# Performance work log

Hardware: AMD Instinct MI355X
Metric: run time of the kernel (lower is better)

## Reference

```python
import jax, jax.numpy as jnp
import numpy as np

N_NODES = 50000
N_EDGES = 800000
D_IN = 128
D_HID = 128
N_CLASSES = 10
N_GRAPHS = 64


def setup_inputs() -> dict:
    key = jax.random.key(0)
    ks = jax.random.split(key, 12)
    x = jax.random.normal(ks[0], (N_NODES, D_IN), dtype=jnp.float32)
    edge_index = jax.random.randint(ks[1], (2, N_EDGES), 0, N_NODES, dtype=jnp.int32)
    batch = jnp.sort(jax.random.randint(ks[2], (N_NODES,), 0, N_GRAPHS, dtype=jnp.int32))
    s = 0.05
    conv0_w = jax.random.normal(ks[3], (D_IN, D_HID), dtype=jnp.float32) * s
    conv0_b = jax.random.normal(ks[4], (D_HID,), dtype=jnp.float32) * s
    conv1_w = jax.random.normal(ks[5], (D_HID, D_HID), dtype=jnp.float32) * s
    conv1_b = jax.random.normal(ks[6], (D_HID,), dtype=jnp.float32) * s
    lin0_w = jax.random.normal(ks[7], (D_HID, D_HID), dtype=jnp.float32) * s
    lin0_b = jax.random.normal(ks[8], (D_HID,), dtype=jnp.float32) * s
    lin1_w = jax.random.normal(ks[9], (D_HID, N_CLASSES), dtype=jnp.float32) * s
    lin1_b = jax.random.normal(ks[10], (N_CLASSES,), dtype=jnp.float32) * s
    return dict(x=x, edge_index=edge_index, batch=batch,
                conv0_w=conv0_w, conv0_b=conv0_b,
                conv1_w=conv1_w, conv1_b=conv1_b,
                lin0_w=lin0_w, lin0_b=lin0_b,
                lin1_w=lin1_w, lin1_b=lin1_b)


def gcn_conv(x, edge_index, w, b):
    # PyG GCNConv: linear transform, add self-loops, D^-1/2 (A+I) D^-1/2 aggregation, + bias
    n = x.shape[0]
    h = x @ w  # [N, out]
    loop = jnp.arange(n, dtype=edge_index.dtype)
    row = jnp.concatenate([edge_index[0], loop])  # source nodes
    col = jnp.concatenate([edge_index[1], loop])  # destination nodes
    deg = jax.ops.segment_sum(jnp.ones_like(col, dtype=h.dtype), col, num_segments=n)
    dinv = jnp.where(deg > 0, jax.lax.rsqrt(deg), 0.0)
    norm = dinv[row] * dinv[col]  # [E+N]
    msg = h[row] * norm[:, None]  # gather + scale
    out = jax.ops.segment_sum(msg, col, num_segments=n)  # scatter-add
    return out + b


def reference(x, edge_index, batch, conv0_w, conv0_b, conv1_w, conv1_b,
              lin0_w, lin0_b, lin1_w, lin1_b):
    h = jax.nn.relu(gcn_conv(x, edge_index, conv0_w, conv0_b))
    h = jax.nn.relu(gcn_conv(h, edge_index, conv1_w, conv1_b))
    # global max pooling over nodes of each graph
    h = jax.ops.segment_max(h, batch, num_segments=N_GRAPHS)  # [G, D_HID]
    # NOTE: original applies relu after EVERY linear, including the output layer
    h = jax.nn.relu(h @ lin0_w + lin0_b)
    h = jax.nn.relu(h @ lin1_w + lin1_b)
    return jax.nn.log_softmax(h, axis=-1)
```

## Files before the change

### kernel.cpp

```cpp
#include <hip/hip_runtime.h>

#define D 128
#define BINCAP 6144
#define P2CAP 6144

typedef __attribute__((ext_vector_type(8))) short short8;
typedef __attribute__((ext_vector_type(4))) float f32x4;
typedef __attribute__((ext_vector_type(2))) float f32x2;

__device__ inline unsigned short f2bf(float f) {
    unsigned u = __float_as_uint(f);
    return (unsigned short)((u + 0x7FFFu + ((u >> 16) & 1u)) >> 16);
}
__device__ inline float bflo(unsigned u) { return __uint_as_float(u << 16); }
__device__ inline float bfhi(unsigned u) { return __uint_as_float(u & 0xFFFF0000u); }

__global__ __launch_bounds__(256) void k_initW(const float* __restrict__ w0, const float* __restrict__ w1,
                                               const float* __restrict__ b0, const float* __restrict__ b1,
                                               uint4* __restrict__ Wp0, uint4* __restrict__ Wp1,
                                               float* __restrict__ b0p, float* __restrict__ b1p,
                                               int* __restrict__ binCur, int* __restrict__ pool,
                                               unsigned* __restrict__ h0b, unsigned* __restrict__ h1b,
                                               int nbins, int n) {
    int t = threadIdx.x, b = blockIdx.x;
    int e = b * 256 + t;
    {
        int l = e & 63, U = (e >> 6) & 7, T = e >> 9;
        int nn = U * 16 + (l & 15);
        int kq = T * 32 + ((l >> 4) << 3);
        unsigned r[4], s[4];
#pragma unroll
        for (int jj = 0; jj < 4; ++jj) {
            int k0 = kq + 2 * jj, k1 = k0 + 1;
            unsigned a0 = f2bf(w0[k0 * 128 + nn]), a1 = f2bf(w0[k1 * 128 + nn]);
            r[jj] = a0 | (a1 << 16);
            int c0 = ((k0 & 7) << 4) | (k0 >> 3), c1 = ((k1 & 7) << 4) | (k1 >> 3);
            unsigned q0 = f2bf(w1[c0 * 128 + nn]), q1 = f2bf(w1[c1 * 128 + nn]);
            s[jj] = q0 | (q1 << 16);
        }
        Wp0[e] = make_uint4(r[0], r[1], r[2], r[3]);
        Wp1[e] = make_uint4(s[0], s[1], s[2], s[3]);
    }
    if (b == 0) {
        if (t < nbins) binCur[t] = t * BINCAP;
        for (int i = t; i < 64 * 128; i += 256) pool[i] = 0;
    }
    if (b == 1 && t < 128) {
        int c = ((t & 7) << 4) | (t >> 3);
        b0p[t] = b0[c];
        b1p[t] = b1[c];
    }
    if (b == 2 && t < 64) {
        h0b[(size_t)n * 64 + t] = 0u;
        h1b[(size_t)n * 64 + t] = 0u;
    }
}

__global__ __launch_bounds__(256) void k_p1scatter(const int* __restrict__ row, const int* __restrict__ col,
                                                   int* __restrict__ binCur, unsigned* __restrict__ ebuf, int E) {
    __shared__ int h[256], delta[256], lcur[256], wt[4];
    __shared__ unsigned stage[4096];
    int t = threadIdx.x;
    int wv = t >> 6, l = t & 63;
    h[t] = 0;
    __syncthreads();
    int base = blockIdx.x * 4096;
    int cnt = min(4096, E - base);
    if (cnt == 4096) {
        int myc[16], myr[16];
        const int4* c4 = (const int4*)(col + base);
        const int4* r4 = (const int4*)(row + base);
#pragma unroll
        for (int k = 0; k < 4; ++k) {
            int4 cv = c4[t * 4 + k];
            int4 rv = r4[t * 4 + k];
            myc[k * 4 + 0] = cv.x; myc[k * 4 + 1] = cv.y; myc[k * 4 + 2] = cv.z; myc[k * 4 + 3] = cv.w;
            myr[k * 4 + 0] = rv.x; myr[k * 4 + 1] = rv.y; myr[k * 4 + 2] = rv.z; myr[k * 4 + 3] = rv.w;
        }
#pragma unroll
        for (int k = 0; k < 16; ++k) atomicAdd(&h[myc[k] >> 8], 1);
        __syncthreads();
        int v = h[t];
        int inc = v;
#pragma unroll
        for (int o = 1; o < 64; o <<= 1) {
            int x = __shfl_up(inc, o, 64);
            if (l >= o) inc += x;
        }
        if (l == 63) wt[wv] = inc;
        __syncthreads();
        int wbase = 0;
#pragma unroll
        for (int j = 0; j < 4; ++j) if (j < wv) wbase += wt[j];
        int excl = wbase + inc - v;
        lcur[t] = excl;
        delta[t] = (v > 0) ? (atomicAdd(&binCur[t], v) - excl) : 0;
        __syncthreads();
#pragma unroll
        for (int k = 0; k < 16; ++k) {
            int d = myc[k];
            int slot = atomicAdd(&lcur[d >> 8], 1);
            stage[slot] = ((unsigned)d << 16) | (unsigned)myr[k];
        }
        __syncthreads();
#pragma unroll
        for (int k = 0; k < 16; ++k) {
            int slot = k * 256 + t;
            unsigned vv = stage[slot];
            int b = vv >> 24;
            ebuf[delta[b] + slot] = vv;
        }
    } else {
        for (int k = 0; k < 16; ++k) {
            int e = base + k * 256 + t;
            if (e < E) atomicAdd(&h[col[e] >> 8], 1);
        }
        __syncthreads();
        int v = h[t];
        int inc = v;
#pragma unroll
        for (int o = 1; o < 64; o <<= 1) {
            int x = __shfl_up(inc, o, 64);
            if (l >= o) inc += x;
        }
        if (l == 63) wt[wv] = inc;
        __syncthreads();
        int wbase = 0;
#pragma unroll
        for (int j = 0; j < 4; ++j) if (j < wv) wbase += wt[j];
        int excl = wbase + inc - v;
        lcur[t] = excl;
        delta[t] = (v > 0) ? (atomicAdd(&binCur[t], v) - excl) : 0;
        __syncthreads();
        for (int k = 0; k < 16; ++k) {
            int e = base + k * 256 + t;
            if (e < E) {
                int d = col[e];
                int slot = atomicAdd(&lcur[d >> 8], 1);
                stage[slot] = ((unsigned)d << 16) | (unsigned)row[e];
            }
        }
        __syncthreads();
        for (int k = 0; k < 16; ++k) {
            int slot = k * 256 + t;
            if (slot < cnt) {
                unsigned vv = stage[slot];
                int b = vv >> 24;
                ebuf[delta[b] + slot] = vv;
            }
        }
    }
}

__global__ __launch_bounds__(256) void k_p2sort(const unsigned* __restrict__ ebuf, const int* __restrict__ binCur,
                                                int* __restrict__ csr, int* __restrict__ off_, int* __restrict__ end_,
                                                float* __restrict__ dinv, int n) {
    __shared__ unsigned stage[P2CAP];
    __shared__ unsigned stage2[P2CAP];
    __shared__ int h[256], cur[256], wt[4];
    int b = blockIdx.x, t = threadIdx.x;
    int wv = t >> 6, l = t & 63;
    int beg = b * BINCAP;
    int cnt = binCur[b] - beg;
    h[t] = 0;
    __syncthreads();
    int nfull = cnt >> 2;
    const uint4* e4 = (const uint4*)(ebuf + beg);
    uint4* st4 = (uint4*)stage;
    for (int i = t; i < nfull; i += 256) {
        uint4 v = e4[i];
        st4[i] = v;
        atomicAdd(&h[(v.x >> 16) & 0xFF], 1);
        atomicAdd(&h[(v.y >> 16) & 0xFF], 1);
        atomicAdd(&h[(v.z >> 16) & 0xFF], 1);
        atomicAdd(&h[(v.w >> 16) & 0xFF], 1);
    }
    for (int i = (nfull << 2) + t; i < cnt; i += 256) {
        unsigned v = ebuf[beg + i];
        stage[i] = v;
        atomicAdd(&h[(v >> 16) & 0xFF], 1);
    }
    __syncthreads();
    int v = h[t];
    int inc = v;
#pragma unroll
    for (int o = 1; o < 64; o <<= 1) {
        int x = __shfl_up(inc, o, 64);
        if (l >= o) inc += x;
    }
    if (l == 63) wt[wv] = inc;
    __syncthreads();
    int wbase = 0;
#pragma unroll
    for (int j = 0; j < 4; ++j) if (j < wv) wbase += wt[j];
    int excl = wbase + inc - v;
    cur[t] = excl;
    int d = b * 256 + t;
    if (d < n) {
        off_[d] = beg + excl;
        end_[d] = beg + excl + v;
        dinv[d] = rsqrtf((float)(v + 1));
    }
    __syncthreads();
    for (int i = t; i < cnt; i += 256) {
        unsigned vv = stage[i];
        int slot = atomicAdd(&cur[(vv >> 16) & 0xFF], 1);
        stage2[slot] = vv & 0xFFFFu;
    }
    __syncthreads();
    uint4* c4o = (uint4*)(csr + beg);
    uint4* st24 = (uint4*)stage2;
    for (int i = t; i < nfull; i += 256) c4o[i] = st24[i];
    for (int i = (nfull << 2) + t; i < cnt; i += 256) csr[beg + i] = (int)stage2[i];
}

__global__ __launch_bounds__(256) void k_gemm0(const float* __restrict__ x, const uint4* __restrict__ Wp,
                                               const float* __restrict__ dinv, unsigned* __restrict__ outb, int n) {
    int wave = threadIdx.x >> 6, l = threadIdx.x & 63;
    int mt = blockIdx.x * 4 + wave;
    int r0 = mt * 16;
    if (r0 >= n) return;
    int rowA = r0 + (l & 15);
    int kq = (l >> 4) * 8;
    f32x4 acc[8];
#pragma unroll
    for (int U = 0; U < 8; ++U) acc[U] = (f32x4){0.f, 0.f, 0.f, 0.f};
    const float* xr = x + (size_t)rowA * 128 + kq;
#pragma unroll
    for (int T = 0; T < 4; ++T) {
        float4 a0 = *(const float4*)(xr + T * 32);
        float4 a1 = *(const float4*)(xr + T * 32 + 4);
        short8 af;
        af[0] = (short)f2bf(a0.x); af[1] = (short)f2bf(a0.y);
        af[2] = (short)f2bf(a0.z); af[3] = (short)f2bf(a0.w);
        af[4] = (short)f2bf(a1.x); af[5] = (short)f2bf(a1.y);
        af[6] = (short)f2bf(a1.z); af[7] = (short)f2bf(a1.w);
#pragma unroll
        for (int U = 0; U < 8; ++U) {
            short8 bf = *(const short8*)&Wp[(T * 8 + U) * 64 + l];
            acc[U] = __builtin_amdgcn_mfma_f32_16x16x32_bf16(af, bf, acc[U], 0, 0, 0);
        }
    }
    int rq = l >> 4, cl = l & 15;
#pragma unroll
    for (int q = 0; q < 4; ++q) {
        int rr = r0 + rq * 4 + q;
        float d = dinv[rr];
        uint4 w;
        w.x = (unsigned)f2bf(acc[0][q] * d) | ((unsigned)f2bf(acc[1][q] * d) << 16);
        w.y = (unsigned)f2bf(acc[2][q] * d) | ((unsigned)f2bf(acc[3][q] * d) << 16);
        w.z = (unsigned)f2bf(acc[4][q] * d) | ((unsigned)f2bf(acc[5][q] * d) << 16);
        w.w = (unsigned)f2bf(acc[6][q] * d) | ((unsigned)f2bf(acc[7][q] * d) << 16);
        *(uint4*)(outb + (size_t)rr * 64 + cl * 4) = w;
    }
}

__device__ inline void gather8(const uint4* __restrict__ hp4, const int* __restrict__ csr,
                               int q, int beg, int len, int ZR, f32x2 acc[4]) {
    int maxlen = len;
    maxlen = max(maxlen, __shfl_xor(maxlen, 16, 64));
    maxlen = max(maxlen, __shfl_xor(maxlen, 32, 64));
    if (maxlen <= 0) return;
    int lm1 = len - 1;
    int s[8];
#pragma unroll
    for (int k = 0; k < 8; ++k) {
        int cv = csr[beg + min(k, lm1)];
        s[k] = (k < len) ? cv : ZR;
    }
    for (int j = 0; j < maxlen; j += 8) {
        uint4 u0 = hp4[(size_t)s[0] * 16 + q];
        uint4 u1 = hp4[(size_t)s[1] * 16 + q];
        uint4 u2 = hp4[(size_t)s[2] * 16 + q];
        uint4 u3 = hp4[(size_t)s[3] * 16 + q];
        uint4 u4 = hp4[(size_t)s[4] * 16 + q];
        uint4 u5 = hp4[(size_t)s[5] * 16 + q];
        uint4 u6 = hp4[(size_t)s[6] * 16 + q];
        uint4 u7 = hp4[(size_t)s[7] * 16 + q];
        int jn = j + 8;
        if (jn < maxlen) {
#pragma unroll
            for (int k = 0; k < 8; ++k) {
                int cv = csr[beg + min(jn + k, lm1)];
                s[k] = (jn + k < len) ? cv : ZR;
            }
        }
#define ACC8(U)                                                     \
        { f32x2 t0, t1, t2, t3;                                     \
          t0[0] = bflo(U.x); t0[1] = bfhi(U.x);                     \
          t1[0] = bflo(U.y); t1[1] = bfhi(U.y);                     \
          t2[0] = bflo(U.z); t2[1] = bfhi(U.z);                     \
          t3[0] = bflo(U.w); t3[1] = bfhi(U.w);                     \
          acc[0] += t0; acc[1] += t1; acc[2] += t2; acc[3] += t3; }
        ACC8(u0) ACC8(u1) ACC8(u2) ACC8(u3)
        ACC8(u4) ACC8(u5) ACC8(u6) ACC8(u7)
#undef ACC8
    }
}

__global__ __launch_bounds__(256) void k_aggemm(const unsigned* __restrict__ hp, const int* __restrict__ off_,
                                                const int* __restrict__ end_, const int* __restrict__ csr,
                                                const float* __restrict__ dinv, const float* __restrict__ bp,
                                                const uint4* __restrict__ Wp, unsigned* __restrict__ outb, int n) {
    __shared__ uint4 sA[16 * 17];
    int w = threadIdx.x >> 6, l = threadIdx.x & 63;
    int g = l >> 4, q = l & 15;
    int r0 = blockIdx.x * 16;
    int node = r0 + w * 4 + g;
    const uint4* hp4 = (const uint4*)hp;
    f32x2 acc[4];
    uint4 us = hp4[(size_t)node * 16 + q];
    acc[0][0] = bflo(us.x); acc[0][1] = bfhi(us.x);
    acc[1][0] = bflo(us.y); acc[1][1] = bfhi(us.y);
    acc[2][0] = bflo(us.z); acc[2][1] = bfhi(us.z);
    acc[3][0] = bflo(us.w); acc[3][1] = bfhi(us.w);
    int beg = off_[node];
    int len = end_[node] - beg;
    gather8(hp4, csr, q, beg, len, n, acc);
    float d0 = dinv[node];
    const float4* bp4 = (const float4*)bp;
    float4 ba = bp4[q * 2], bb = bp4[q * 2 + 1];
    uint4 pk;
    pk.x = (unsigned)f2bf(fmaxf(fmaf(d0, acc[0][0], ba.x), 0.f)) | ((unsigned)f2bf(fmaxf(fmaf(d0, acc[0][1], ba.y), 0.f)) << 16);
    pk.y = (unsigned)f2bf(fmaxf(fmaf(d0, acc[1][0], ba.z), 0.f)) | ((unsigned)f2bf(fmaxf(fmaf(d0, acc[1][1], ba.w), 0.f)) << 16);
    pk.z = (unsigned)f2bf(fmaxf(fmaf(d0, acc[2][0], bb.x), 0.f)) | ((unsigned)f2bf(fmaxf(fmaf(d0, acc[2][1], bb.y), 0.f)) << 16);
    pk.w = (unsigned)f2bf(fmaxf(fmaf(d0, acc[3][0], bb.z), 0.f)) | ((unsigned)f2bf(fmaxf(fmaf(d0, acc[3][1], bb.w), 0.f)) << 16);
    sA[(w * 4 + g) * 17 + q] = pk;
    __syncthreads();
    int rq = l >> 4, cl = l & 15;
    f32x4 c0v = (f32x4){0.f, 0.f, 0.f, 0.f}, c1v = (f32x4){0.f, 0.f, 0.f, 0.f};
#pragma unroll
    for (int T = 0; T < 4; ++T) {
        short8 af = *(const short8*)&sA[(l & 15) * 17 + T * 4 + rq];
        short8 bf0 = *(const short8*)&Wp[(T * 8 + 2 * w) * 64 + l];
        short8 bf1 = *(const short8*)&Wp[(T * 8 + 2 * w + 1) * 64 + l];
        c0v = __builtin_amdgcn_mfma_f32_16x16x32_bf16(af, bf0, c0v, 0, 0, 0);
        c1v = __builtin_amdgcn_mfma_f32_16x16x32_bf16(af, bf1, c1v, 0, 0, 0);
    }
#pragma unroll
    for (int qq = 0; qq < 4; ++qq) {
        int rr = r0 + rq * 4 + qq;
        float d2 = dinv[rr];
        unsigned pkk = (unsigned)f2bf(c0v[qq] * d2) | ((unsigned)f2bf(c1v[qq] * d2) << 16);
        outb[(size_t)rr * 64 + cl * 4 + w] = pkk;
    }
}

__global__ __launch_bounds__(256) void k_agg1(const unsigned* __restrict__ hp, const int* __restrict__ off_,
                                              const int* __restrict__ end_, const int* __restrict__ csr,
                                              const float* __restrict__ dinv, const float* __restrict__ bp,
                                              const int* __restrict__ batch, int* __restrict__ pool, int n) {
    __shared__ float2 sv[16][64];
    __shared__ int sg[16];
    int w = threadIdx.x >> 6, l = threadIdx.x & 63;
    int g = l >> 4, q = l & 15;
    int node = blockIdx.x * 16 + w * 4 + g;
    const uint4* hp4 = (const uint4*)hp;
    f32x2 acc[4];
    uint4 us = hp4[(size_t)node * 16 + q];
    acc[0][0] = bflo(us.x); acc[0][1] = bfhi(us.x);
    acc[1][0] = bflo(us.y); acc[1][1] = bfhi(us.y);
    acc[2][0] = bflo(us.z); acc[2][1] = bfhi(us.z);
    acc[3][0] = bflo(us.w); acc[3][1] = bfhi(us.w);
    int beg = off_[node];
    int len = end_[node] - beg;
    gather8(hp4, csr, q, beg, len, n, acc);
    float d0 = dinv[node];
    const float4* bp4 = (const float4*)bp;
    float4 ba = bp4[q * 2], bb = bp4[q * 2 + 1];
    int rowi = w * 4 + g;
    sv[rowi][q * 4 + 0] = make_float2(fmaxf(fmaf(d0, acc[0][0], ba.x), 0.f), fmaxf(fmaf(d0, acc[0][1], ba.y), 0.f));
    sv[rowi][q * 4 + 1] = make_float2(fmaxf(fmaf(d0, acc[1][0], ba.z), 0.f), fmaxf(fmaf(d0, acc[1][1], ba.w), 0.f));
    sv[rowi][q * 4 + 2] = make_float2(fmaxf(fmaf(d0, acc[2][0], bb.x), 0.f), fmaxf(fmaf(d0, acc[2][1], bb.y), 0.f));
    sv[rowi][q * 4 + 3] = make_float2(fmaxf(fmaf(d0, acc[3][0], bb.z), 0.f), fmaxf(fmaf(d0, acc[3][1], bb.w), 0.f));
    if (q == 0) sg[rowi] = batch[node];
    __syncthreads();
    if (threadIdx.x < 64) {
        int t = threadIdx.x;
        int c0 = 32 * (t & 3) + (t >> 2);
        int cur = sg[0];
        float2 m = sv[0][t];
        for (int ww = 1; ww < 16; ++ww) {
            int gg = sg[ww];
            float2 vv = sv[ww][t];
            if (gg == cur) { m.x = fmaxf(m.x, vv.x); m.y = fmaxf(m.y, vv.y); }
            else {
                atomicMax(&pool[cur * 128 + c0], __float_as_int(m.x));
                atomicMax(&pool[cur * 128 + c0 + 16], __float_as_int(m.y));
                cur = gg; m = vv;
            }
        }
        atomicMax(&pool[cur * 128 + c0], __float_as_int(m.x));
        atomicMax(&pool[cur * 128 + c0 + 16], __float_as_int(m.y));
    }
}

__global__ __launch_bounds__(128) void k_mlp(const float* __restrict__ pool, const float* __restrict__ W0,
                                             const float* __restrict__ b0, const float* __restrict__ W1,
                                             const float* __restrict__ b1, float* __restrict__ out) {
    __shared__ float rowv[128];
    __shared__ float h2[128];
    __shared__ float ps[80];
    __shared__ float h3[10];
    __shared__ float lsed;
    int g = blockIdx.x, t = threadIdx.x;
    rowv[t] = pool[g * 128 + t];
    __syncthreads();
    float acc = b0[t];
    for (int k = 0; k < 128; ++k) acc = fmaf(rowv[k], W0[k * 128 + t], acc);
    h2[t] = fmaxf(acc, 0.f);
    __syncthreads();
    if (t < 80) {
        int j = t >> 3, p = t & 7;
        float a = 0.f;
        int k0 = p * 16;
        for (int k = k0; k < k0 + 16; ++k) a = fmaf(h2[k], W1[k * 10 + j], a);
        ps[t] = a;
    }
    __syncthreads();
    if (t < 10) {
        float a = b1[t];
#pragma unroll
        for (int p = 0; p < 8; ++p) a += ps[t * 8 + p];
        h3[t] = fmaxf(a, 0.f);
    }
    __syncthreads();
    if (t == 0) {
        float mx = h3[0];
        for (int j = 1; j < 10; ++j) mx = fmaxf(mx, h3[j]);
        float s = 0.f;
        for (int j = 0; j < 10; ++j) s += expf(h3[j] - mx);
        lsed = logf(s) + mx;
    }
    __syncthreads();
    if (t < 10) out[g * 10 + t] = h3[t] - lsed;
}

extern "C" void kernel_launch(void* const* d_in, const int* in_sizes, int n_in,
                              void* d_out, int out_size, void* d_ws, size_t ws_size,
                              hipStream_t stream) {
    const float* x   = (const float*)d_in[0];
    const int* eidx  = (const int*)d_in[1];
    const int* batch = (const int*)d_in[2];
    const float* w0  = (const float*)d_in[3];
    const float* b0  = (const float*)d_in[4];
    const float* w1  = (const float*)d_in[5];
    const float* b1  = (const float*)d_in[6];
    const float* lw0 = (const float*)d_in[7];
    const float* lb0 = (const float*)d_in[8];
    const float* lw1 = (const float*)d_in[9];
    const float* lb1 = (const float*)d_in[10];
    float* out = (float*)d_out;

    int n = in_sizes[2];
    int E = in_sizes[1] / 2;
    const int* row = eidx;
    const int* col = eidx + E;
    int nbins = (n + 255) >> 8;
    int nb1 = (E + 4095) / 4096;

    char* ws = (char*)d_ws;
    size_t o = 0;
    auto take = [&](size_t bytes) { void* p = ws + o; o += (bytes + 255) & ~(size_t)255; return p; };
    int*      binCur   = (int*)     take(256 * 4);
    int*      off_     = (int*)     take((size_t)n * 4);
    int*      end_     = (int*)     take((size_t)n * 4);
    float*    dinv     = (float*)   take((size_t)n * 4);
    int*      csrA     = (int*)     take(((size_t)nbins * BINCAP + 128) * 4);
    int*      csr      = csrA + 64;
    unsigned* ebuf     = (unsigned*)take(((size_t)nbins * BINCAP + 64) * 4);
    uint4*    Wp0      = (uint4*)   take(2048 * 16);
    uint4*    Wp1      = (uint4*)   take(2048 * 16);
    float*    b0p      = (float*)   take(128 * 4);
    float*    b1p      = (float*)   take(128 * 4);
    unsigned* h0b      = (unsigned*)take((size_t)(n + 1) * 64 * 4);
    unsigned* h1b      = (unsigned*)take((size_t)(n + 1) * 64 * 4);
    int*      pool     = (int*)     take(64 * 128 * 4);

    k_initW<<<8, 256, 0, stream>>>(w0, w1, b0, b1, Wp0, Wp1, b0p, b1p, binCur, pool, h0b, h1b, nbins, n);
    k_p1scatter<<<nb1, 256, 0, stream>>>(row, col, binCur, ebuf, E);
    k_p2sort<<<nbins, 256, 0, stream>>>(ebuf, binCur, csr, off_, end_, dinv, n);

    int mtBlocks = ((n + 15) / 16 + 3) / 4;

    k_gemm0<<<mtBlocks, 256, 0, stream>>>(x, Wp0, dinv, h0b, n);
    k_aggemm<<<n / 16, 256, 0, stream>>>(h0b, off_, end_, csr, dinv, b0p, Wp1, h1b, n);
    k_agg1<<<n / 16, 256, 0, stream>>>(h1b, off_, end_, csr, dinv, b1p, batch, pool, n);
    k_mlp<<<64, 128, 0, stream>>>((const float*)pool, lw0, lb0, lw1, lb1, out);
}
```

Baseline: 178.9 us.

## Store intermediate node features as per-row int8 with scale for gathers

Intermediate hidden features are now stored as per-row, absmax-scaled unsigned int8 values with a +128 offset and one float scale per row, replacing bf16. The gather kernels dequantise with an FMA per element and apply an offset correction from the summed scales. Gathered row bytes drop from 256 to 128 per node, which targets the memory traffic of the random edge gathers. The cost is extra quantisation arithmetic, an extra scale load per neighbour, an additional shared-memory pass and barrier in the fused aggregate-GEMM kernel, and reduced numerical precision.

```diff
diff --git a/kernel.cpp b/kernel.cpp
--- a/kernel.cpp
+++ b/kernel.cpp
@@ -12,15 +12,14 @@
     unsigned u = __float_as_uint(f);
     return (unsigned short)((u + 0x7FFFu + ((u >> 16) & 1u)) >> 16);
 }
-__device__ inline float bflo(unsigned u) { return __uint_as_float(u << 16); }
-__device__ inline float bfhi(unsigned u) { return __uint_as_float(u & 0xFFFF0000u); }
 
 __global__ __launch_bounds__(256) void k_initW(const float* __restrict__ w0, const float* __restrict__ w1,
                                                const float* __restrict__ b0, const float* __restrict__ b1,
                                                uint4* __restrict__ Wp0, uint4* __restrict__ Wp1,
                                                float* __restrict__ b0p, float* __restrict__ b1p,
                                                int* __restrict__ binCur, int* __restrict__ pool,
-                                               unsigned* __restrict__ h0b, unsigned* __restrict__ h1b,
+                                               uint2* __restrict__ rows0, float* __restrict__ scl0,
+                                               uint2* __restrict__ rows1, float* __restrict__ scl1,
                                                int nbins, int n) {
     int t = threadIdx.x, b = blockIdx.x;
     int e = b * 256 + t;
@@ -50,9 +49,10 @@
         b0p[t] = b0[c];
         b1p[t] = b1[c];
     }
-    if (b == 2 && t < 64) {
-        h0b[(size_t)n * 64 + t] = 0u;
-        h1b[(size_t)n * 64 + t] = 0u;
+    if (b == 2) {
+        if (t < 16) rows0[(size_t)n * 16 + t] = make_uint2(0u, 0u);
+        if (t < 16) rows1[(size_t)n * 16 + t] = make_uint2(0u, 0u);
+        if (t == 0) { scl0[n] = 0.f; scl1[n] = 0.f; }
     }
 }
 
@@ -215,7 +215,8 @@
 }
 
 __global__ __launch_bounds__(256) void k_gemm0(const float* __restrict__ x, const uint4* __restrict__ Wp,
-                                               const float* __restrict__ dinv, unsigned* __restrict__ outb, int n) {
+                                               const float* __restrict__ dinv,
+                                               uint2* __restrict__ rows0, float* __restrict__ scl0, int n) {
     int wave = threadIdx.x >> 6, l = threadIdx.x & 63;
     int mt = blockIdx.x * 4 + wave;
     int r0 = mt * 16;
@@ -243,20 +244,32 @@
     }
     int rq = l >> 4, cl = l & 15;
 #pragma unroll
-    for (int q = 0; q < 4; ++q) {
-        int rr = r0 + rq * 4 + q;
+    for (int qq = 0; qq < 4; ++qq) {
+        int rr = r0 + rq * 4 + qq;
         float d = dinv[rr];
-        uint4 w;
-        w.x = (unsigned)f2bf(acc[0][q] * d) | ((unsigned)f2bf(acc[1][q] * d) << 16);
-        w.y = (unsigned)f2bf(acc[2][q] * d) | ((unsigned)f2bf(acc[3][q] * d) << 16);
-        w.z = (unsigned)f2bf(acc[4][q] * d) | ((unsigned)f2bf(acc[5][q] * d) << 16);
-        w.w = (unsigned)f2bf(acc[6][q] * d) | ((unsigned)f2bf(acc[7][q] * d) << 16);
-        *(uint4*)(outb + (size_t)rr * 64 + cl * 4) = w;
-    }
-}
-
-__device__ inline void gather8(const uint4* __restrict__ hp4, const int* __restrict__ csr,
-                               int q, int beg, int len, int ZR, f32x2 acc[4]) {
+        float v[8];
+        float am = 0.f;
+#pragma unroll
+        for (int U = 0; U < 8; ++U) { v[U] = acc[U][qq] * d; am = fmaxf(am, fabsf(v[U])); }
+        am = fmaxf(am, __shfl_xor(am, 1, 64));
+        am = fmaxf(am, __shfl_xor(am, 2, 64));
+        am = fmaxf(am, __shfl_xor(am, 4, 64));
+        am = fmaxf(am, __shfl_xor(am, 8, 64));
+        float inv = (am > 0.f) ? 127.f / am : 0.f;
+        unsigned bb[8];
+#pragma unroll
+        for (int U = 0; U < 8; ++U) bb[U] = (unsigned)(__float2int_rn(v[U] * inv) + 128);
+        uint2 o;
+        o.x = bb[0] | (bb[1] << 8) | (bb[2] << 16) | (bb[3] << 24);
+        o.y = bb[4] | (bb[5] << 8) | (bb[6] << 16) | (bb[7] << 24);
+        rows0[(size_t)rr * 16 + cl] = o;
+        if (cl == 0) scl0[rr] = am * (1.f / 127.f);
+    }
+}
+
+__device__ inline void gather8q(const uint2* __restrict__ rows, const float* __restrict__ scl,
+                                const int* __restrict__ csr, int q, int beg, int len, int ZR,
+                                f32x2 acc[4], float& ssum) {
     int maxlen = len;
     maxlen = max(maxlen, __shfl_xor(maxlen, 16, 64));
     maxlen = max(maxlen, __shfl_xor(maxlen, 32, 64));
@@ -269,14 +282,13 @@
         s[k] = (k < len) ? cv : ZR;
     }
     for (int j = 0; j < maxlen; j += 8) {
-        uint4 u0 = hp4[(size_t)s[0] * 16 + q];
-        uint4 u1 = hp4[(size_t)s[1] * 16 + q];
-        uint4 u2 = hp4[(size_t)s[2] * 16 + q];
-        uint4 u3 = hp4[(size_t)s[3] * 16 + q];
-        uint4 u4 = hp4[(size_t)s[4] * 16 + q];
-        uint4 u5 = hp4[(size_t)s[5] * 16 + q];
-        uint4 u6 = hp4[(size_t)s[6] * 16 + q];
-        uint4 u7 = hp4[(size_t)s[7] * 16 + q];
+        uint2 u[8];
+        float sc[8];
+#pragma unroll
+        for (int k = 0; k < 8; ++k) {
+            u[k] = rows[(size_t)s[k] * 16 + q];
+            sc[k] = scl[s[k]];
+        }
         int jn = j + 8;
         if (jn < maxlen) {
 #pragma unroll
@@ -285,46 +297,65 @@
                 s[k] = (jn + k < len) ? cv : ZR;
             }
         }
-#define ACC8(U)                                                     \
-        { f32x2 t0, t1, t2, t3;                                     \
-          t0[0] = bflo(U.x); t0[1] = bfhi(U.x);                     \
-          t1[0] = bflo(U.y); t1[1] = bfhi(U.y);                     \
-          t2[0] = bflo(U.z); t2[1] = bfhi(U.z);                     \
-          t3[0] = bflo(U.w); t3[1] = bfhi(U.w);                     \
-          acc[0] += t0; acc[1] += t1; acc[2] += t2; acc[3] += t3; }
-        ACC8(u0) ACC8(u1) ACC8(u2) ACC8(u3)
-        ACC8(u4) ACC8(u5) ACC8(u6) ACC8(u7)
-#undef ACC8
-    }
-}
-
-__global__ __launch_bounds__(256) void k_aggemm(const unsigned* __restrict__ hp, const int* __restrict__ off_,
-                                                const int* __restrict__ end_, const int* __restrict__ csr,
-                                                const float* __restrict__ dinv, const float* __restrict__ bp,
-                                                const uint4* __restrict__ Wp, unsigned* __restrict__ outb, int n) {
+#pragma unroll
+        for (int k = 0; k < 8; ++k) {
+            float f = sc[k];
+            unsigned vx = u[k].x, vy = u[k].y;
+            acc[0][0] = fmaf((float)(vx & 0xFFu),         f, acc[0][0]);
+            acc[0][1] = fmaf((float)((vx >> 8) & 0xFFu),  f, acc[0][1]);
+            acc[1][0] = fmaf((float)((vx >> 16) & 0xFFu), f, acc[1][0]);
+            acc[1][1] = fmaf((float)(vx >> 24),           f, acc[1][1]);
+            acc[2][0] = fmaf((float)(vy & 0xFFu),         f, acc[2][0]);
+            acc[2][1] = fmaf((float)((vy >> 8) & 0xFFu),  f, acc[2][1]);
+            acc[3][0] = fmaf((float)((vy >> 16) & 0xFFu), f, acc[3][0]);
+            acc[3][1] = fmaf((float)(vy >> 24),           f, acc[3][1]);
+            ssum += f;
+        }
+    }
+}
+
+__global__ __launch_bounds__(256) void k_aggemm(const uint2* __restrict__ rows0, const float* __restrict__ scl0,
+                                                const int* __restrict__ off_, const int* __restrict__ end_,
+                                                const int* __restrict__ csr, const float* __restrict__ dinv,
+                                                const float* __restrict__ bp, const uint4* __restrict__ Wp,
+                                                uint2* __restrict__ rows1, float* __restrict__ scl1, int n) {
     __shared__ uint4 sA[16 * 17];
+    __shared__ float sM[4][16];
+    __shared__ unsigned short sPB[16][64];
     int w = threadIdx.x >> 6, l = threadIdx.x & 63;
     int g = l >> 4, q = l & 15;
     int r0 = blockIdx.x * 16;
     int node = r0 + w * 4 + g;
-    const uint4* hp4 = (const uint4*)hp;
     f32x2 acc[4];
-    uint4 us = hp4[(size_t)node * 16 + q];
-    acc[0][0] = bflo(us.x); acc[0][1] = bfhi(us.x);
-    acc[1][0] = bflo(us.y); acc[1][1] = bfhi(us.y);
-    acc[2][0] = bflo(us.z); acc[2][1] = bfhi(us.z);
-    acc[3][0] = bflo(us.w); acc[3][1] = bfhi(us.w);
+#pragma unroll
+    for (int j = 0; j < 4; ++j) { acc[j][0] = 0.f; acc[j][1] = 0.f; }
+    float ssum;
+    {
+        uint2 us = rows0[(size_t)node * 16 + q];
+        float f = scl0[node];
+        unsigned vx = us.x, vy = us.y;
+        acc[0][0] = fmaf((float)(vx & 0xFFu),         f, acc[0][0]);
+        acc[0][1] = fmaf((float)((vx >> 8) & 0xFFu),  f, acc[0][1]);
+        acc[1][0] = fmaf((float)((vx >> 16) & 0xFFu), f, acc[1][0]);
+        acc[1][1] = fmaf((float)(vx >> 24),           f, acc[1][1]);
+        acc[2][0] = fmaf((float)(vy & 0xFFu),         f, acc[2][0]);
+        acc[2][1] = fmaf((float)((vy >> 8) & 0xFFu),  f, acc[2][1]);
+        acc[3][0] = fmaf((float)((vy >> 16) & 0xFFu), f, acc[3][0]);
+        acc[3][1] = fmaf((float)(vy >> 24),           f, acc[3][1]);
+        ssum = f;
+    }
     int beg = off_[node];
     int len = end_[node] - beg;
-    gather8(hp4, csr, q, beg, len, n, acc);
+    gather8q(rows0, scl0, csr, q, beg, len, n, acc, ssum);
+    float corr = -128.f * ssum;
     float d0 = dinv[node];
     const float4* bp4 = (const float4*)bp;
     float4 ba = bp4[q * 2], bb = bp4[q * 2 + 1];
     uint4 pk;
-    pk.x = (unsigned)f2bf(fmaxf(fmaf(d0, acc[0][0], ba.x), 0.f)) | ((unsigned)f2bf(fmaxf(fmaf(d0, acc[0][1], ba.y), 0.f)) << 16);
-    pk.y = (unsigned)f2bf(fmaxf(fmaf(d0, acc[1][0], ba.z), 0.f)) | ((unsigned)f2bf(fmaxf(fmaf(d0, acc[1][1], ba.w), 0.f)) << 16);
-    pk.z = (unsigned)f2bf(fmaxf(fmaf(d0, acc[2][0], bb.x), 0.f)) | ((unsigned)f2bf(fmaxf(fmaf(d0, acc[2][1], bb.y), 0.f)) << 16);
-    pk.w = (unsigned)f2bf(fmaxf(fmaf(d0, acc[3][0], bb.z), 0.f)) | ((unsigned)f2bf(fmaxf(fmaf(d0, acc[3][1], bb.w), 0.f)) << 16);
+    pk.x = (unsigned)f2bf(fmaxf(fmaf(d0, acc[0][0] + corr, ba.x), 0.f)) | ((unsigned)f2bf(fmaxf(fmaf(d0, acc[0][1] + corr, ba.y), 0.f)) << 16);
+    pk.y = (unsigned)f2bf(fmaxf(fmaf(d0, acc[1][0] + corr, ba.z), 0.f)) | ((unsigned)f2bf(fmaxf(fmaf(d0, acc[1][1] + corr, ba.w), 0.f)) << 16);
+    pk.z = (unsigned)f2bf(fmaxf(fmaf(d0, acc[2][0] + corr, bb.x), 0.f)) | ((unsigned)f2bf(fmaxf(fmaf(d0, acc[2][1] + corr, bb.y), 0.f)) << 16);
+    pk.w = (unsigned)f2bf(fmaxf(fmaf(d0, acc[3][0] + corr, bb.z), 0.f)) | ((unsigned)f2bf(fmaxf(fmaf(d0, acc[3][1] + corr, bb.w), 0.f)) << 16);
     sA[(w * 4 + g) * 17 + q] = pk;
     __syncthreads();
     int rq = l >> 4, cl = l & 15;
@@ -337,42 +368,85 @@
         c0v = __builtin_amdgcn_mfma_f32_16x16x32_bf16(af, bf0, c0v, 0, 0, 0);
         c1v = __builtin_amdgcn_mfma_f32_16x16x32_bf16(af, bf1, c1v, 0, 0, 0);
     }
+    float cq0[4], cq1[4], am01[4];
 #pragma unroll
     for (int qq = 0; qq < 4; ++qq) {
         int rr = r0 + rq * 4 + qq;
         float d2 = dinv[rr];
-        unsigned pkk = (unsigned)f2bf(c0v[qq] * d2) | ((unsigned)f2bf(c1v[qq] * d2) << 16);
-        outb[(size_t)rr * 64 + cl * 4 + w] = pkk;
-    }
-}
-
-__global__ __launch_bounds__(256) void k_agg1(const unsigned* __restrict__ hp, const int* __restrict__ off_,
-                                              const int* __restrict__ end_, const int* __restrict__ csr,
-                                              const float* __restrict__ dinv, const float* __restrict__ bp,
-                                              const int* __restrict__ batch, int* __restrict__ pool, int n) {
+        cq0[qq] = c0v[qq] * d2;
+        cq1[qq] = c1v[qq] * d2;
+        float am = fmaxf(fabsf(cq0[qq]), fabsf(cq1[qq]));
+        am = fmaxf(am, __shfl_xor(am, 1, 64));
+        am = fmaxf(am, __shfl_xor(am, 2, 64));
+        am = fmaxf(am, __shfl_xor(am, 4, 64));
+        am = fmaxf(am, __shfl_xor(am, 8, 64));
+        am01[qq] = am;
+    }
+    if (cl == 0) {
+#pragma unroll
+        for (int qq = 0; qq < 4; ++qq) sM[w][rq * 4 + qq] = am01[qq];
+    }
+    __syncthreads();
+#pragma unroll
+    for (int qq = 0; qq < 4; ++qq) {
+        int rw = rq * 4 + qq;
+        float m = fmaxf(fmaxf(sM[0][rw], sM[1][rw]), fmaxf(sM[2][rw], sM[3][rw]));
+        float inv = (m > 0.f) ? 127.f / m : 0.f;
+        unsigned q0 = (unsigned)(__float2int_rn(cq0[qq] * inv) + 128);
+        unsigned q1 = (unsigned)(__float2int_rn(cq1[qq] * inv) + 128);
+        sPB[rw][cl * 4 + w] = (unsigned short)(q0 | (q1 << 8));
+        if (w == 0 && cl == 0) scl1[r0 + rw] = m * (1.f / 127.f);
+    }
+    __syncthreads();
+    {
+        int r = threadIdx.x >> 4, L = threadIdx.x & 15;
+        uint2 o;
+        o.x = (unsigned)sPB[r][4 * L + 0] | ((unsigned)sPB[r][4 * L + 1] << 16);
+        o.y = (unsigned)sPB[r][4 * L + 2] | ((unsigned)sPB[r][4 * L + 3] << 16);
+        rows1[(size_t)(r0 + r) * 16 + L] = o;
+    }
+}
+
+__global__ __launch_bounds__(256) void k_agg1(const uint2* __restrict__ rows1, const float* __restrict__ scl1,
+                                              const int* __restrict__ off_, const int* __restrict__ end_,
+                                              const int* __restrict__ csr, const float* __restrict__ dinv,
+                                              const float* __restrict__ bp, const int* __restrict__ batch,
+                                              int* __restrict__ pool, int n) {
     __shared__ float2 sv[16][64];
     __shared__ int sg[16];
     int w = threadIdx.x >> 6, l = threadIdx.x & 63;
     int g = l >> 4, q = l & 15;
     int node = blockIdx.x * 16 + w * 4 + g;
-    const uint4* hp4 = (const uint4*)hp;
     f32x2 acc[4];
-    uint4 us = hp4[(size_t)node * 16 + q];
-    acc[0][0] = bflo(us.x); acc[0][1] = bfhi(us.x);
-    acc[1][0] = bflo(us.y); acc[1][1] = bfhi(us.y);
-    acc[2][0] = bflo(us.z); acc[2][1] = bfhi(us.z);
-    acc[3][0] = bflo(us.w); acc[3][1] = bfhi(us.w);
+#pragma unroll
+    for (int j = 0; j < 4; ++j) { acc[j][0] = 0.f; acc[j][1] = 0.f; }
+    float ssum;
+    {
+        uint2 us = rows1[(size_t)node * 16 + q];
+        float f = scl1[node];
+        unsigned vx = us.x, vy = us.y;
+        acc[0][0] = fmaf((float)(vx & 0xFFu),         f, acc[0][0]);
+        acc[0][1] = fmaf((float)((vx >> 8) & 0xFFu),  f, acc[0][1]);
+        acc[1][0] = fmaf((float)((vx >> 16) & 0xFFu), f, acc[1][0]);
+        acc[1][1] = fmaf((float)(vx >> 24),           f, acc[1][1]);
+        acc[2][0] = fmaf((float)(vy & 0xFFu),         f, acc[2][0]);
+        acc[2][1] = fmaf((float)((vy >> 8) & 0xFFu),  f, acc[2][1]);
+        acc[3][0] = fmaf((float)((vy >> 16) & 0xFFu), f, acc[3][0]);
+        acc[3][1] = fmaf((float)(vy >> 24),           f, acc[3][1]);
+        ssum = f;
+    }
     int beg = off_[node];
     int len = end_[node] - beg;
-    gather8(hp4, csr, q, beg, len, n, acc);
+    gather8q(rows1, scl1, csr, q, beg, len, n, acc, ssum);
+    float corr = -128.f * ssum;
     float d0 = dinv[node];
     const float4* bp4 = (const float4*)bp;
     float4 ba = bp4[q * 2], bb = bp4[q * 2 + 1];
     int rowi = w * 4 + g;
-    sv[rowi][q * 4 + 0] = make_float2(fmaxf(fmaf(d0, acc[0][0], ba.x), 0.f), fmaxf(fmaf(d0, acc[0][1], ba.y), 0.f));
-    sv[rowi][q * 4 + 1] = make_float2(fmaxf(fmaf(d0, acc[1][0], ba.z), 0.f), fmaxf(fmaf(d0, acc[1][1], ba.w), 0.f));
-    sv[rowi][q * 4 + 2] = make_float2(fmaxf(fmaf(d0, acc[2][0], bb.x), 0.f), fmaxf(fmaf(d0, acc[2][1], bb.y), 0.f));
-    sv[rowi][q * 4 + 3] = make_float2(fmaxf(fmaf(d0, acc[3][0], bb.z), 0.f), fmaxf(fmaf(d0, acc[3][1], bb.w), 0.f));
+    sv[rowi][q * 4 + 0] = make_float2(fmaxf(fmaf(d0, acc[0][0] + corr, ba.x), 0.f), fmaxf(fmaf(d0, acc[0][1] + corr, ba.y), 0.f));
+    sv[rowi][q * 4 + 1] = make_float2(fmaxf(fmaf(d0, acc[1][0] + corr, ba.z), 0.f), fmaxf(fmaf(d0, acc[1][1] + corr, ba.w), 0.f));
+    sv[rowi][q * 4 + 2] = make_float2(fmaxf(fmaf(d0, acc[2][0] + corr, bb.x), 0.f), fmaxf(fmaf(d0, acc[2][1] + corr, bb.y), 0.f));
+    sv[rowi][q * 4 + 3] = make_float2(fmaxf(fmaf(d0, acc[3][0] + corr, bb.z), 0.f), fmaxf(fmaf(d0, acc[3][1] + corr, bb.w), 0.f));
     if (q == 0) sg[rowi] = batch[node];
     __syncthreads();
     if (threadIdx.x < 64) {
@@ -473,18 +547,21 @@
     uint4*    Wp1      = (uint4*)   take(2048 * 16);
     float*    b0p      = (float*)   take(128 * 4);
     float*    b1p      = (float*)   take(128 * 4);
-    unsigned* h0b      = (unsigned*)take((size_t)(n + 1) * 64 * 4);
-    unsigned* h1b      = (unsigned*)take((size_t)(n + 1) * 64 * 4);
+    uint2*    rows0    = (uint2*)   take((size_t)(n + 1) * 128);
+    float*    scl0     = (float*)   take((size_t)(n + 1) * 4);
+    uint2*    rows1    = (uint2*)   take((size_t)(n + 1) * 128);
+    float*    scl1     = (float*)   take((size_t)(n + 1) * 4);
     int*      pool     = (int*)     take(64 * 128 * 4);
 
-    k_initW<<<8, 256, 0, stream>>>(w0, w1, b0, b1, Wp0, Wp1, b0p, b1p, binCur, pool, h0b, h1b, nbins, n);
+    k_initW<<<8, 256, 0, stream>>>(w0, w1, b0, b1, Wp0, Wp1, b0p, b1p, binCur, pool,
+                                   rows0, scl0, rows1, scl1, nbins, n);
     k_p1scatter<<<nb1, 256, 0, stream>>>(row, col, binCur, ebuf, E);
     k_p2sort<<<nbins, 256, 0, stream>>>(ebuf, binCur, csr, off_, end_, dinv, n);
 
     int mtBlocks = ((n + 15) / 16 + 3) / 4;
 
-    k_gemm0<<<mtBlocks, 256, 0, stream>>>(x, Wp0, dinv, h0b, n);
-    k_aggemm<<<n / 16, 256, 0, stream>>>(h0b, off_, end_, csr, dinv, b0p, Wp1, h1b, n);
-    k_agg1<<<n / 16, 256, 0, stream>>>(h1b, off_, end_, csr, dinv, b1p, batch, pool, n);
+    k_gemm0<<<mtBlocks, 256, 0, stream>>>(x, Wp0, dinv, rows0, scl0, n);
+    k_aggemm<<<n / 16, 256, 0, stream>>>(rows0, scl0, off_, end_, csr, dinv, b0p, Wp1, rows1, scl1, n);
+    k_agg1<<<n / 16, 256, 0, stream>>>(rows1, scl1, off_, end_, csr, dinv, b1p, batch, pool, n);
     k_mlp<<<64, 128, 0, stream>>>((const float*)pool, lw0, lb0, lw1, lb1, out);
 }
```

Measured after the change: 167.6 us, median of 2. 6.3% less time.
